# Kernel tuning notes

Hardware: AMD Instinct MI355X
Metric: run time of the kernel (lower is better)

The kernel has to match this reference:

```python
import jax, jax.numpy as jnp
import numpy as np

N = 100000      # nodes
E = 1600000     # edges (avg degree 16)
EP = 500000     # pos/neg scored edges
DIN, DH, DOUT = 128, 128, 64


def setup_inputs() -> dict:
    key = jax.random.key(0)
    ks = jax.random.split(key, 8)
    x = jax.random.normal(ks[0], (N, DIN), jnp.float32)
    edge_index = jax.random.randint(ks[1], (2, E), 0, N)
    pos_edge_index = jax.random.randint(ks[2], (2, EP), 0, N)
    neg_edge_index = jax.random.randint(ks[3], (2, EP), 0, N)
    s = lambda k, sh: jax.random.normal(k, sh, jnp.float32) * 0.05
    return dict(
        x=x, edge_index=edge_index,
        pos_edge_index=pos_edge_index, neg_edge_index=neg_edge_index,
        W_l0=s(ks[4], (DIN, DH)), b_l0=jnp.zeros((DH,), jnp.float32), W_r0=s(ks[5], (DIN, DH)),
        W_l1=s(ks[6], (DH, DOUT)), b_l1=jnp.zeros((DOUT,), jnp.float32), W_r1=s(ks[7], (DH, DOUT)),
    )


def sage_conv(h, src, dst, W_l, b_l, W_r):
    # PyG SAGEConv (mean aggr): out_i = W_l @ mean_{j in N(i)} h_j + b_l + W_r @ h_i
    msg = h[src]                                                   # [E, d] gather
    agg = jax.ops.segment_sum(msg, dst, num_segments=h.shape[0])   # [N, d]
    deg = jax.ops.segment_sum(jnp.ones((src.shape[0],), h.dtype), dst, num_segments=h.shape[0])
    mean = agg / jnp.maximum(deg, 1.0)[:, None]
    return mean @ W_l + b_l + h @ W_r


def reference(x, edge_index, pos_edge_index, neg_edge_index,
              W_l0, b_l0, W_r0, W_l1, b_l1, W_r1):
    src, dst = edge_index[0], edge_index[1]
    h = sage_conv(x, src, dst, W_l0, b_l0, W_r0)
    h = jax.nn.relu(h)          # dropout is identity in eval mode
    h = sage_conv(h, src, dst, W_l1, b_l1, W_r1)
    pos_scores = (h[pos_edge_index[0]] * h[pos_edge_index[1]]).sum(axis=1)
    neg_scores = (h[neg_edge_index[0]] * h[neg_edge_index[1]]).sum(axis=1)
    return (pos_scores, neg_scores)
```

## Files before the change

### kernel.cpp

```cpp
#include <hip/hip_runtime.h>

#define NN 100000
#define EE 1600000
#define EPE 500000
#define NBINS 196
#define BCAP 12288
#define EPB 2048
#define NB1 782
#define GEMMB 782
#define CONVB 6250

typedef short bf8_t __attribute__((ext_vector_type(8)));
typedef float f4_t  __attribute__((ext_vector_type(4)));
typedef float f2v  __attribute__((ext_vector_type(2)));

__device__ __forceinline__ unsigned short f2bf(float f) {
    unsigned u = __float_as_uint(f);
    unsigned r = (u + 0x7fffu + ((u >> 16) & 1u)) >> 16;
    return (unsigned short)r;
}
__device__ __forceinline__ float bfl(unsigned u) { return __uint_as_float(u << 16); }
__device__ __forceinline__ float bfh(unsigned u) { return __uint_as_float(u & 0xffff0000u); }

__device__ __forceinline__ int c0p(int m) {
    return ((m >> 6) & 1) * 64 + (m & 3) * 16 + ((m >> 2) & 15);
}
__device__ __forceinline__ int c1p(int m) {
    return ((m >> 5) & 1) * 32 + (m & 1) * 16 + ((m >> 1) & 15);
}

#if __has_builtin(__builtin_amdgcn_cvt_pk_fp8_f32) && __has_builtin(__builtin_amdgcn_cvt_pk_f32_fp8)
__device__ __forceinline__ unsigned pk4_fp8(float a0, float a1, float a2, float a3) {
    int w = 0;
    w = __builtin_amdgcn_cvt_pk_fp8_f32(a0, a1, w, false);
    w = __builtin_amdgcn_cvt_pk_fp8_f32(a2, a3, w, true);
    return (unsigned)w;
}
__device__ __forceinline__ unsigned short pk2_fp8(float a0, float a1) {
    int w = __builtin_amdgcn_cvt_pk_fp8_f32(a0, a1, 0, false);
    return (unsigned short)(w & 0xffff);
}
__device__ __forceinline__ void accf8(float* a, uint2 v) {
    f2v p0 = __builtin_amdgcn_cvt_pk_f32_fp8((int)v.x, false);
    f2v p1 = __builtin_amdgcn_cvt_pk_f32_fp8((int)v.x, true);
    f2v p2 = __builtin_amdgcn_cvt_pk_f32_fp8((int)v.y, false);
    f2v p3 = __builtin_amdgcn_cvt_pk_f32_fp8((int)v.y, true);
    a[0] += p0.x; a[1] += p0.y; a[2] += p1.x; a[3] += p1.y;
    a[4] += p2.x; a[5] += p2.y; a[6] += p3.x; a[7] += p3.y;
}
#else
#include <hip/hip_fp8.h>
__device__ __forceinline__ unsigned pk4_fp8(float a0, float a1, float a2, float a3) {
    unsigned r;
    r  = (unsigned)__hip_cvt_float_to_fp8(a0, __HIP_SATFINITE, __HIP_E4M3);
    r |= (unsigned)__hip_cvt_float_to_fp8(a1, __HIP_SATFINITE, __HIP_E4M3) << 8;
    r |= (unsigned)__hip_cvt_float_to_fp8(a2, __HIP_SATFINITE, __HIP_E4M3) << 16;
    r |= (unsigned)__hip_cvt_float_to_fp8(a3, __HIP_SATFINITE, __HIP_E4M3) << 24;
    return r;
}
__device__ __forceinline__ unsigned short pk2_fp8(float a0, float a1) {
    unsigned r;
    r  = (unsigned)__hip_cvt_float_to_fp8(a0, __HIP_SATFINITE, __HIP_E4M3);
    r |= (unsigned)__hip_cvt_float_to_fp8(a1, __HIP_SATFINITE, __HIP_E4M3) << 8;
    return (unsigned short)r;
}
__device__ __forceinline__ float dec1_fp8(unsigned b) {
    __hip_fp8_e4m3 h; h.__x = (__hip_fp8_storage_t)(b & 0xff);
    return (float)h;
}
__device__ __forceinline__ void accf8(float* a, uint2 v) {
    a[0] += dec1_fp8(v.x); a[1] += dec1_fp8(v.x >> 8);
    a[2] += dec1_fp8(v.x >> 16); a[3] += dec1_fp8(v.x >> 24);
    a[4] += dec1_fp8(v.y); a[5] += dec1_fp8(v.y >> 8);
    a[6] += dec1_fp8(v.y >> 16); a[7] += dec1_fp8(v.y >> 24);
}
#endif

__device__ void binpass1_body(int blk, const int* __restrict__ src,
                              const int* __restrict__ dst,
                              int* __restrict__ bin_cnt, int* __restrict__ binbuf)
{
    __shared__ int cnt_l[NBINS];
    __shared__ int base_l[NBINS];
    int tid = threadIdx.x;
    int e0 = blk * EPB;
    for (int i = tid; i < NBINS; i += 256) cnt_l[i] = 0;
    __syncthreads();

    int pk[8];
    #pragma unroll
    for (int i = 0; i < 8; ++i) {
        int e = e0 + tid + i * 256;
        pk[i] = -1;
        if (e < EE) {
            int d = dst[e];
            int b = d >> 9;
            int r = atomicAdd(&cnt_l[b], 1);
            pk[i] = (b << 20) | ((d & 511) << 11) | r;
        }
    }
    __syncthreads();
    for (int i = tid; i < NBINS; i += 256)
        base_l[i] = atomicAdd(&bin_cnt[i], cnt_l[i]);
    __syncthreads();

    #pragma unroll
    for (int i = 0; i < 8; ++i) {
        int e = e0 + tid + i * 256;
        if (e >= EE) continue;
        int v = pk[i];
        int b = v >> 20, dl = (v >> 11) & 511, r = v & 2047;
        binbuf[b * BCAP + base_l[b] + r] = (dl << 17) | src[e];
    }
}

__device__ void binpass2_body(int b, const int* __restrict__ binbuf,
                              const int* __restrict__ bin_cnt, int* __restrict__ csr,
                              int* __restrict__ row_ptr, float* __restrict__ invd)
{
    __shared__ int deg_l[512];
    __shared__ int off_l[512];
    __shared__ int cur_l[512];
    __shared__ int s[256];
    int tid = threadIdx.x;
    int lo = b << 9;
    int n_here = min(512, NN - lo);

    int bc = (tid < NBINS) ? bin_cnt[tid] : 0;
    s[tid] = bc;
    __syncthreads();
    #pragma unroll
    for (int off = 1; off < 256; off <<= 1) {
        int t = (tid >= off) ? s[tid - off] : 0;
        __syncthreads();
        s[tid] += t;
        __syncthreads();
    }
    int base = (b == 0) ? 0 : s[b - 1];
    int cnt = bin_cnt[b];
    const int* bb = binbuf + b * BCAP;
    __syncthreads();

    deg_l[tid] = 0; deg_l[tid + 256] = 0;
    __syncthreads();
    for (int i = tid; i < cnt; i += 256)
        atomicAdd(&deg_l[bb[i] >> 17], 1);
    __syncthreads();

    int a0 = deg_l[2 * tid], a1 = deg_l[2 * tid + 1];
    s[tid] = a0 + a1;
    __syncthreads();
    #pragma unroll
    for (int off = 1; off < 256; off <<= 1) {
        int t = (tid >= off) ? s[tid - off] : 0;
        __syncthreads();
        s[tid] += t;
        __syncthreads();
    }
    int excl = s[tid] - (a0 + a1);
    off_l[2 * tid] = excl;
    off_l[2 * tid + 1] = excl + a0;
    cur_l[2 * tid] = excl;
    cur_l[2 * tid + 1] = excl + a0;
    __syncthreads();

    for (int j = tid; j < n_here; j += 256) {
        row_ptr[lo + j] = base + off_l[j];
        invd[lo + j] = 1.0f / fmaxf((float)deg_l[j], 1.0f);
    }
    if (tid == 0 && b == NBINS - 1) row_ptr[NN] = EE;

    for (int i = tid; i < cnt; i += 256) {
        int v = bb[i];
        int dstl = v >> 17, srcv = v & 0x1FFFF;
        int pos = atomicAdd(&cur_l[dstl], 1);
        csr[base + pos] = srcv;
    }
}

__device__ void pack_body(int blk, const float* __restrict__ Wl0, const float* __restrict__ Wr0,
                          const float* __restrict__ Wl1, const float* __restrict__ Wr1,
                          const float* __restrict__ bl0, const float* __restrict__ bl1,
                          unsigned short* __restrict__ Bp0, unsigned short* __restrict__ Bp1,
                          float* __restrict__ b0p, float* __restrict__ b1p)
{
    int t = blk * 256 + threadIdx.x;
    if (t < 4096) {
        int q = t & 3;
        int n = (t >> 2) & 255;
        int kt = t >> 10;
        unsigned short o[8];
        #pragma unroll
        for (int j = 0; j < 8; ++j) {
            int k = kt * 32 + q * 8 + j;
            float v = (n < 128) ? Wl0[(size_t)k * 128 + n] : Wr0[(size_t)k * 128 + (n - 128)];
            o[j] = f2bf(v);
        }
        uint4 w;
        w.x = (unsigned)o[0] | ((unsigned)o[1] << 16);
        w.y = (unsigned)o[2] | ((unsigned)o[3] << 16);
        w.z = (unsigned)o[4] | ((unsigned)o[5] << 16);
        w.w = (unsigned)o[6] | ((unsigned)o[7] << 16);
        *(uint4*)(Bp0 + (size_t)t * 8) = w;
    } else if (t < 6144) {
        int u = t - 4096;
        int q = u & 3;
        int n = (u >> 2) & 127;
        int kt = u >> 9;
        unsigned short o[8];
        #pragma unroll
        for (int j = 0; j < 8; ++j) {
            int k = kt * 32 + q * 8 + j;
            int c = c0p(k);
            float v = (n < 64) ? Wl1[(size_t)c * 64 + n] : Wr1[(size_t)c * 64 + (n - 64)];
            o[j] = f2bf(v);
        }
        uint4 w;
        w.x = (unsigned)o[0] | ((unsigned)o[1] << 16);
        w.y = (unsigned)o[2] | ((unsigned)o[3] << 16);
        w.z = (unsigned)o[4] | ((unsigned)o[5] << 16);
        w.w = (unsigned)o[6] | ((unsigned)o[7] << 16);
        *(uint4*)(Bp1 + (size_t)u * 8) = w;
    } else if (t < 6144 + 128) {
        int m = t - 6144;
        b0p[m] = bl0[c0p(m)];
    } else if (t < 6144 + 192) {
        int m = t - 6272;
        b1p[m] = bl1[c1p(m)];
    }
}

__device__ void conv_body(int blk, const float* __restrict__ x, unsigned short* __restrict__ xb)
{
    int i = blk * 256 + threadIdx.x;
    const float4* xp = (const float4*)x + (size_t)i * 2;
    float4 a = xp[0], b = xp[1];
    uint4 w;
    w.x = (unsigned)f2bf(a.x) | ((unsigned)f2bf(a.y) << 16);
    w.y = (unsigned)f2bf(a.z) | ((unsigned)f2bf(a.w) << 16);
    w.z = (unsigned)f2bf(b.x) | ((unsigned)f2bf(b.y) << 16);
    w.w = (unsigned)f2bf(b.z) | ((unsigned)f2bf(b.w) << 16);
    *(uint4*)(xb + (size_t)i * 8) = w;
}

template<int NCOLS>
__device__ __forceinline__ void gemm_body(
    int blk, const unsigned short* __restrict__ Ab, const unsigned short* __restrict__ Bp,
    unsigned char* __restrict__ Tout, unsigned short* __restrict__ Rout)
{
    constexpr int STRIP = NCOLS / 4;
    constexpr int NT = STRIP / 16;
    constexpr int HC = NCOLS / 2;
    int w = threadIdx.x >> 6;
    int lane = threadIdx.x & 63;
    int ln = lane & 15, q = lane >> 4;
    int half = w >> 1, wsub = w & 1;
    int row0 = blk * 128;
    int colbase = half * HC + wsub * STRIP;

    bf8_t Bf[4][NT];
    #pragma unroll
    for (int kt = 0; kt < 4; ++kt)
        #pragma unroll
        for (int nt = 0; nt < NT; ++nt)
            Bf[kt][nt] = *(const bf8_t*)(Bp + (size_t)kt * NCOLS * 32
                                         + (size_t)(colbase + nt * 16 + ln) * 32 + q * 8);

    #pragma unroll
    for (int rt = 0; rt < 8; ++rt) {
        int rowt = row0 + rt * 16;
        if (rowt < NN) {
            int arow = rowt + ln;
            bf8_t Af[4];
            #pragma unroll
            for (int kt = 0; kt < 4; ++kt)
                Af[kt] = *(const bf8_t*)(Ab + (size_t)arow * 128 + kt * 32 + q * 8);

            f4_t acc[NT];
            #pragma unroll
            for (int nt = 0; nt < NT; ++nt) acc[nt] = (f4_t){0.f, 0.f, 0.f, 0.f};
            #pragma unroll
            for (int kt = 0; kt < 4; ++kt)
                #pragma unroll
                for (int nt = 0; nt < NT; ++nt)
                    acc[nt] = __builtin_amdgcn_mfma_f32_16x16x32_bf16(Af[kt], Bf[kt][nt], acc[nt], 0, 0, 0);

            #pragma unroll
            for (int r = 0; r < 4; ++r) {
                int row = rowt + q * 4 + r;
                if (half == 0) {
                    if (NT == 4) {
                        unsigned v = pk4_fp8(acc[0][r], acc[1][r], acc[2][r], acc[3][r]);
                        *(unsigned*)(Tout + (size_t)row * HC + wsub * 64 + ln * 4) = v;
                    } else {
                        unsigned short v = pk2_fp8(acc[0][r], acc[1][r]);
                        *(unsigned short*)(Tout + (size_t)row * HC + wsub * 32 + ln * 2) = v;
                    }
                } else {
                    if (NT == 4) {
                        uint2 v;
                        v.x = (unsigned)f2bf(acc[0][r]) | ((unsigned)f2bf(acc[1][r]) << 16);
                        v.y = (unsigned)f2bf(acc[2][r]) | ((unsigned)f2bf(acc[3][r]) << 16);
                        *(uint2*)(Rout + (size_t)row * HC + wsub * 64 + ln * 4) = v;
                    } else {
                        unsigned v = (unsigned)f2bf(acc[0][r]) | ((unsigned)f2bf(acc[1][r]) << 16);
                        *(unsigned*)(Rout + (size_t)row * HC + wsub * 32 + ln * 2) = v;
                    }
                }
            }
        }
    }
}

__global__ __launch_bounds__(256) void prep_k(
    const int* __restrict__ src, const int* __restrict__ dst,
    int* __restrict__ bin_cnt, int* __restrict__ binbuf,
    const float* __restrict__ x, unsigned short* __restrict__ xb,
    const float* __restrict__ Wl0, const float* __restrict__ Wr0,
    const float* __restrict__ Wl1, const float* __restrict__ Wr1,
    const float* __restrict__ bl0, const float* __restrict__ bl1,
    unsigned short* __restrict__ Bp0, unsigned short* __restrict__ Bp1,
    float* __restrict__ b0p, float* __restrict__ b1p)
{
    if (blockIdx.x < NB1)
        binpass1_body(blockIdx.x, src, dst, bin_cnt, binbuf);
    else if (blockIdx.x < NB1 + 25)
        pack_body(blockIdx.x - NB1, Wl0, Wr0, Wl1, Wr1, bl0, bl1, Bp0, Bp1, b0p, b1p);
    else
        conv_body(blockIdx.x - NB1 - 25, x, xb);
}

__global__ __launch_bounds__(256) void gemm0_bp2_k(
    const unsigned short* __restrict__ xb, const unsigned short* __restrict__ Bp0,
    unsigned char* __restrict__ t0q, unsigned short* __restrict__ r0b,
    const int* __restrict__ binbuf, const int* __restrict__ bin_cnt,
    int* __restrict__ csr, int* __restrict__ row_ptr, float* __restrict__ invd)
{
    if (blockIdx.x < GEMMB)
        gemm_body<256>(blockIdx.x, xb, Bp0, t0q, r0b);
    else
        binpass2_body(blockIdx.x - GEMMB, binbuf, bin_cnt, csr, row_ptr, invd);
}

__global__ __launch_bounds__(256) void gemm1_k(
    const unsigned short* __restrict__ h1b, const unsigned short* __restrict__ Bp1,
    unsigned char* __restrict__ t1q, unsigned short* __restrict__ r1b)
{
    gemm_body<128>(blockIdx.x, h1b, Bp1, t1q, r1b);
}

__device__ __forceinline__ void unp8(float* a, uint4 v) {
    a[0] = bfl(v.x); a[1] = bfh(v.x);
    a[2] = bfl(v.y); a[3] = bfh(v.y);
    a[4] = bfl(v.z); a[5] = bfh(v.z);
    a[6] = bfl(v.w); a[7] = bfh(v.w);
}

template<int LPNS, bool RELU>
__global__ __launch_bounds__(256) void gather_fuse_k(
    const unsigned char* __restrict__ tq, const int* __restrict__ csr,
    const int* __restrict__ row_ptr, const float* __restrict__ invd,
    const unsigned short* __restrict__ rg, const float* __restrict__ biasp,
    unsigned short* __restrict__ hout)
{
    constexpr int STRIDE = 8 << LPNS;
    int t = blockIdx.x * 256 + threadIdx.x;
    int node = t >> LPNS;
    int lane = t & ((1 << LPNS) - 1);
    if (node >= NN) return;
    int e = row_ptr[node];
    int e1 = row_ptr[node + 1];
    const unsigned char* fb = tq + lane * 8;

    float a0[8] = {0.f, 0.f, 0.f, 0.f, 0.f, 0.f, 0.f, 0.f};
    float a1[8] = {0.f, 0.f, 0.f, 0.f, 0.f, 0.f, 0.f, 0.f};
    for (; e + 3 < e1; e += 4) {
        int s0 = csr[e], s1 = csr[e + 1], s2 = csr[e + 2], s3 = csr[e + 3];
        uint2 v0 = *(const uint2*)(fb + (size_t)s0 * STRIDE);
        uint2 v1 = *(const uint2*)(fb + (size_t)s1 * STRIDE);
        uint2 v2 = *(const uint2*)(fb + (size_t)s2 * STRIDE);
        uint2 v3 = *(const uint2*)(fb + (size_t)s3 * STRIDE);
        accf8(a0, v0); accf8(a1, v1); accf8(a0, v2); accf8(a1, v3);
    }
    for (; e < e1; ++e) {
        int s0 = csr[e];
        uint2 v0 = *(const uint2*)(fb + (size_t)s0 * STRIDE);
        accf8(a0, v0);
    }

    float inv = invd[node];
    uint4 rv = *(const uint4*)(rg + (size_t)node * STRIDE + lane * 8);
    float rr[8];
    unp8(rr, rv);
    f4_t b0 = *(const f4_t*)(biasp + lane * 8);
    f4_t b1 = *(const f4_t*)(biasp + lane * 8 + 4);
    float o[8];
    #pragma unroll
    for (int j = 0; j < 8; ++j) {
        float bj = (j < 4) ? b0[j] : b1[j - 4];
        float v = (a0[j] + a1[j]) * inv + rr[j] + bj;
        o[j] = RELU ? fmaxf(v, 0.f) : v;
    }
    uint4 w;
    w.x = (unsigned)f2bf(o[0]) | ((unsigned)f2bf(o[1]) << 16);
    w.y = (unsigned)f2bf(o[2]) | ((unsigned)f2bf(o[3]) << 16);
    w.z = (unsigned)f2bf(o[4]) | ((unsigned)f2bf(o[5]) << 16);
    w.w = (unsigned)f2bf(o[6]) | ((unsigned)f2bf(o[7]) << 16);
    *(uint4*)(hout + (size_t)node * STRIDE + lane * 8) = w;
}

__device__ __forceinline__ float dot8(uint4 va, uint4 vb) {
    return bfl(va.x) * bfl(vb.x) + bfh(va.x) * bfh(vb.x)
         + bfl(va.y) * bfl(vb.y) + bfh(va.y) * bfh(vb.y)
         + bfl(va.z) * bfl(vb.z) + bfh(va.z) * bfh(vb.z)
         + bfl(va.w) * bfl(vb.w) + bfh(va.w) * bfh(vb.w);
}

__global__ __launch_bounds__(256) void score_k(
    const unsigned short* __restrict__ h2b, const int* __restrict__ pos,
    const int* __restrict__ neg, float* __restrict__ out)
{
    int t = blockIdx.x * 256 + threadIdx.x;
    int g = t >> 3, l = t & 7;
    int eg0 = g * 2;
    if (eg0 >= 2 * EPE) return;
    int eg1 = eg0 + 1;
    int a0i, b0i, a1i, b1i;
    if (eg0 < EPE) { a0i = pos[eg0]; b0i = pos[EPE + eg0]; }
    else { int e2 = eg0 - EPE; a0i = neg[e2]; b0i = neg[EPE + e2]; }
    if (eg1 < EPE) { a1i = pos[eg1]; b1i = pos[EPE + eg1]; }
    else { int e2 = eg1 - EPE; a1i = neg[e2]; b1i = neg[EPE + e2]; }
    const unsigned short* hb = h2b + (size_t)l * 8;
    uint4 va0 = *(const uint4*)(hb + (size_t)a0i * 64);
    uint4 vb0 = *(const uint4*)(hb + (size_t)b0i * 64);
    uint4 va1 = *(const uint4*)(hb + (size_t)a1i * 64);
    uint4 vb1 = *(const uint4*)(hb + (size_t)b1i * 64);
    float p0 = dot8(va0, vb0);
    float p1 = dot8(va1, vb1);
    p0 += __shfl_xor(p0, 1, 8);
    p1 += __shfl_xor(p1, 1, 8);
    p0 += __shfl_xor(p0, 2, 8);
    p1 += __shfl_xor(p1, 2, 8);
    p0 += __shfl_xor(p0, 4, 8);
    p1 += __shfl_xor(p1, 4, 8);
    if (l == 0) { out[eg0] = p0; out[eg1] = p1; }
}

extern "C" void kernel_launch(void* const* d_in, const int* in_sizes, int n_in,
                              void* d_out, int out_size, void* d_ws, size_t ws_size,
                              hipStream_t stream) {
    const float* x   = (const float*)d_in[0];
    const int*   ei  = (const int*)d_in[1];
    const int*   pei = (const int*)d_in[2];
    const int*   nei = (const int*)d_in[3];
    const float* Wl0 = (const float*)d_in[4];
    const float* bl0 = (const float*)d_in[5];
    const float* Wr0 = (const float*)d_in[6];
    const float* Wl1 = (const float*)d_in[7];
    const float* bl1 = (const float*)d_in[8];
    const float* Wr1 = (const float*)d_in[9];
    float* out = (float*)d_out;

    char* ws = (char*)d_ws;
    size_t off = 0;
    auto alloc = [&](size_t bytes) {
        void* p = ws + off;
        off = (off + bytes + 255) & ~(size_t)255;
        return p;
    };
    float* invd     = (float*)alloc((size_t)NN * 4);
    int*   row_ptr  = (int*)  alloc((size_t)(NN + 1) * 4);
    int*   bin_cnt  = (int*)  alloc((size_t)NBINS * 4);
    int*   binbuf   = (int*)  alloc((size_t)NBINS * BCAP * 4);
    int*   csr      = (int*)  alloc((size_t)EE * 4);
    unsigned short* Bp0 = (unsigned short*)alloc((size_t)4096 * 8 * 2);
    unsigned short* Bp1 = (unsigned short*)alloc((size_t)2048 * 8 * 2);
    float* b0p = (float*)alloc(128 * 4);
    float* b1p = (float*)alloc(64 * 4);
    unsigned short* xb  = (unsigned short*)alloc((size_t)NN * 128 * 2);
    unsigned char*  t0q = (unsigned char*) alloc((size_t)NN * 128);
    unsigned short* r0b = (unsigned short*)alloc((size_t)NN * 128 * 2);
    unsigned short* h1b = (unsigned short*)alloc((size_t)NN * 128 * 2);
    unsigned char*  t1q = t0q;
    unsigned short* r1b = r0b;
    unsigned short* h2b = h1b;

    const int* src = ei;
    const int* dst = ei + EE;

    hipMemsetAsync(bin_cnt, 0, (size_t)NBINS * 4, stream);

    prep_k<<<NB1 + 25 + CONVB, 256, 0, stream>>>(
        src, dst, bin_cnt, binbuf, x, xb,
        Wl0, Wr0, Wl1, Wr1, bl0, bl1, Bp0, Bp1, b0p, b1p);

    gemm0_bp2_k<<<GEMMB + NBINS, 256, 0, stream>>>(
        xb, Bp0, t0q, r0b, binbuf, bin_cnt, csr, row_ptr, invd);

    gather_fuse_k<4, true><<<(NN * 16 + 255) / 256, 256, 0, stream>>>(
        t0q, csr, row_ptr, invd, r0b, b0p, h1b);

    gemm1_k<<<GEMMB, 256, 0, stream>>>(h1b, Bp1, t1q, r1b);

    gather_fuse_k<3, false><<<(NN * 8 + 255) / 256, 256, 0, stream>>>(
        t1q, csr, row_ptr, invd, r1b, b1p, h2b);

    score_k<<<(EPE * 8 + 255) / 256, 256, 0, stream>>>(h2b, pei, nei, out);
}
```

Baseline: 284.3 us.

## Widen per-thread work in gather, binning and bf16 conversion kernels

The gather-fuse kernel now has each thread handle 16 features with 16-byte fp8 loads instead of 8 features with 8-byte loads. That halves the threads per node and the redundant CSR index reads, and makes each gather load wider. The binning pass now processes 4096 edges per block with a wider rank field, and the x-to-bf16 conversion handles 32 elements per thread, which shrinks the grid sizes. In exchange, per-thread register use rises, which can lower occupancy and latency hiding for the irregular gathers.

```diff
diff --git a/kernel.cpp b/kernel.cpp
--- a/kernel.cpp
+++ b/kernel.cpp
@@ -5,10 +5,10 @@
 #define EPE 500000
 #define NBINS 196
 #define BCAP 12288
-#define EPB 2048
-#define NB1 782
+#define EPB 4096
+#define NB1 391
 #define GEMMB 782
-#define CONVB 6250
+#define CONVB 1563
 
 typedef short bf8_t __attribute__((ext_vector_type(8)));
 typedef float f4_t  __attribute__((ext_vector_type(4)));
@@ -40,11 +40,11 @@
     int w = __builtin_amdgcn_cvt_pk_fp8_f32(a0, a1, 0, false);
     return (unsigned short)(w & 0xffff);
 }
-__device__ __forceinline__ void accf8(float* a, uint2 v) {
-    f2v p0 = __builtin_amdgcn_cvt_pk_f32_fp8((int)v.x, false);
-    f2v p1 = __builtin_amdgcn_cvt_pk_f32_fp8((int)v.x, true);
-    f2v p2 = __builtin_amdgcn_cvt_pk_f32_fp8((int)v.y, false);
-    f2v p3 = __builtin_amdgcn_cvt_pk_f32_fp8((int)v.y, true);
+__device__ __forceinline__ void accf8(float* a, unsigned lo, unsigned hi) {
+    f2v p0 = __builtin_amdgcn_cvt_pk_f32_fp8((int)lo, false);
+    f2v p1 = __builtin_amdgcn_cvt_pk_f32_fp8((int)lo, true);
+    f2v p2 = __builtin_amdgcn_cvt_pk_f32_fp8((int)hi, false);
+    f2v p3 = __builtin_amdgcn_cvt_pk_f32_fp8((int)hi, true);
     a[0] += p0.x; a[1] += p0.y; a[2] += p1.x; a[3] += p1.y;
     a[4] += p2.x; a[5] += p2.y; a[6] += p3.x; a[7] += p3.y;
 }
@@ -68,11 +68,11 @@
     __hip_fp8_e4m3 h; h.__x = (__hip_fp8_storage_t)(b & 0xff);
     return (float)h;
 }
-__device__ __forceinline__ void accf8(float* a, uint2 v) {
-    a[0] += dec1_fp8(v.x); a[1] += dec1_fp8(v.x >> 8);
-    a[2] += dec1_fp8(v.x >> 16); a[3] += dec1_fp8(v.x >> 24);
-    a[4] += dec1_fp8(v.y); a[5] += dec1_fp8(v.y >> 8);
-    a[6] += dec1_fp8(v.y >> 16); a[7] += dec1_fp8(v.y >> 24);
+__device__ __forceinline__ void accf8(float* a, unsigned lo, unsigned hi) {
+    a[0] += dec1_fp8(lo); a[1] += dec1_fp8(lo >> 8);
+    a[2] += dec1_fp8(lo >> 16); a[3] += dec1_fp8(lo >> 24);
+    a[4] += dec1_fp8(hi); a[5] += dec1_fp8(hi >> 8);
+    a[6] += dec1_fp8(hi >> 16); a[7] += dec1_fp8(hi >> 24);
 }
 #endif
 
@@ -87,16 +87,16 @@
     for (int i = tid; i < NBINS; i += 256) cnt_l[i] = 0;
     __syncthreads();
 
-    int pk[8];
-    #pragma unroll
-    for (int i = 0; i < 8; ++i) {
+    int pk[16];
+    #pragma unroll
+    for (int i = 0; i < 16; ++i) {
         int e = e0 + tid + i * 256;
         pk[i] = -1;
         if (e < EE) {
             int d = dst[e];
             int b = d >> 9;
             int r = atomicAdd(&cnt_l[b], 1);
-            pk[i] = (b << 20) | ((d & 511) << 11) | r;
+            pk[i] = (b << 21) | ((d & 511) << 12) | r;
         }
     }
     __syncthreads();
@@ -105,11 +105,11 @@
     __syncthreads();
 
     #pragma unroll
-    for (int i = 0; i < 8; ++i) {
+    for (int i = 0; i < 16; ++i) {
         int e = e0 + tid + i * 256;
         if (e >= EE) continue;
         int v = pk[i];
-        int b = v >> 20, dl = (v >> 11) & 511, r = v & 2047;
+        int b = v >> 21, dl = (v >> 12) & 511, r = v & 4095;
         binbuf[b * BCAP + base_l[b] + r] = (dl << 17) | src[e];
     }
 }
@@ -233,14 +233,22 @@
 __device__ void conv_body(int blk, const float* __restrict__ x, unsigned short* __restrict__ xb)
 {
     int i = blk * 256 + threadIdx.x;
-    const float4* xp = (const float4*)x + (size_t)i * 2;
-    float4 a = xp[0], b = xp[1];
-    uint4 w;
-    w.x = (unsigned)f2bf(a.x) | ((unsigned)f2bf(a.y) << 16);
-    w.y = (unsigned)f2bf(a.z) | ((unsigned)f2bf(a.w) << 16);
-    w.z = (unsigned)f2bf(b.x) | ((unsigned)f2bf(b.y) << 16);
-    w.w = (unsigned)f2bf(b.z) | ((unsigned)f2bf(b.w) << 16);
-    *(uint4*)(xb + (size_t)i * 8) = w;
+    if (i >= (NN * 128) / 32) return;
+    const float4* xp = (const float4*)x + (size_t)i * 8;
+    float4 v[8];
+    #pragma unroll
+    for (int j = 0; j < 8; ++j) v[j] = xp[j];
+    uint4* op = (uint4*)(xb + (size_t)i * 32);
+    #pragma unroll
+    for (int j = 0; j < 4; ++j) {
+        float4 a = v[2 * j], b = v[2 * j + 1];
+        uint4 w;
+        w.x = (unsigned)f2bf(a.x) | ((unsigned)f2bf(a.y) << 16);
+        w.y = (unsigned)f2bf(a.z) | ((unsigned)f2bf(a.w) << 16);
+        w.z = (unsigned)f2bf(b.x) | ((unsigned)f2bf(b.y) << 16);
+        w.w = (unsigned)f2bf(b.z) | ((unsigned)f2bf(b.w) << 16);
+        op[j] = w;
+    }
 }
 
 template<int NCOLS>
@@ -356,57 +364,69 @@
     a[6] = bfl(v.w); a[7] = bfh(v.w);
 }
 
-template<int LPNS, bool RELU>
+template<int LPNS2, bool RELU>
 __global__ __launch_bounds__(256) void gather_fuse_k(
     const unsigned char* __restrict__ tq, const int* __restrict__ csr,
     const int* __restrict__ row_ptr, const float* __restrict__ invd,
     const unsigned short* __restrict__ rg, const float* __restrict__ biasp,
     unsigned short* __restrict__ hout)
 {
-    constexpr int STRIDE = 8 << LPNS;
+    constexpr int ROW = 16 << LPNS2;
     int t = blockIdx.x * 256 + threadIdx.x;
-    int node = t >> LPNS;
-    int lane = t & ((1 << LPNS) - 1);
+    int node = t >> LPNS2;
+    int lane = t & ((1 << LPNS2) - 1);
     if (node >= NN) return;
     int e = row_ptr[node];
     int e1 = row_ptr[node + 1];
-    const unsigned char* fb = tq + lane * 8;
-
-    float a0[8] = {0.f, 0.f, 0.f, 0.f, 0.f, 0.f, 0.f, 0.f};
-    float a1[8] = {0.f, 0.f, 0.f, 0.f, 0.f, 0.f, 0.f, 0.f};
+    const unsigned char* fb = tq + lane * 16;
+
+    float a0[16], a1[16];
+    #pragma unroll
+    for (int j = 0; j < 16; ++j) { a0[j] = 0.f; a1[j] = 0.f; }
+
     for (; e + 3 < e1; e += 4) {
         int s0 = csr[e], s1 = csr[e + 1], s2 = csr[e + 2], s3 = csr[e + 3];
-        uint2 v0 = *(const uint2*)(fb + (size_t)s0 * STRIDE);
-        uint2 v1 = *(const uint2*)(fb + (size_t)s1 * STRIDE);
-        uint2 v2 = *(const uint2*)(fb + (size_t)s2 * STRIDE);
-        uint2 v3 = *(const uint2*)(fb + (size_t)s3 * STRIDE);
-        accf8(a0, v0); accf8(a1, v1); accf8(a0, v2); accf8(a1, v3);
+        uint4 v0 = *(const uint4*)(fb + (size_t)s0 * ROW);
+        uint4 v1 = *(const uint4*)(fb + (size_t)s1 * ROW);
+        uint4 v2 = *(const uint4*)(fb + (size_t)s2 * ROW);
+        uint4 v3 = *(const uint4*)(fb + (size_t)s3 * ROW);
+        accf8(a0, v0.x, v0.y); accf8(a0 + 8, v0.z, v0.w);
+        accf8(a1, v1.x, v1.y); accf8(a1 + 8, v1.z, v1.w);
+        accf8(a0, v2.x, v2.y); accf8(a0 + 8, v2.z, v2.w);
+        accf8(a1, v3.x, v3.y); accf8(a1 + 8, v3.z, v3.w);
     }
     for (; e < e1; ++e) {
         int s0 = csr[e];
-        uint2 v0 = *(const uint2*)(fb + (size_t)s0 * STRIDE);
-        accf8(a0, v0);
+        uint4 v0 = *(const uint4*)(fb + (size_t)s0 * ROW);
+        accf8(a0, v0.x, v0.y); accf8(a0 + 8, v0.z, v0.w);
     }
 
     float inv = invd[node];
-    uint4 rv = *(const uint4*)(rg + (size_t)node * STRIDE + lane * 8);
-    float rr[8];
-    unp8(rr, rv);
-    f4_t b0 = *(const f4_t*)(biasp + lane * 8);
-    f4_t b1 = *(const f4_t*)(biasp + lane * 8 + 4);
-    float o[8];
-    #pragma unroll
-    for (int j = 0; j < 8; ++j) {
-        float bj = (j < 4) ? b0[j] : b1[j - 4];
-        float v = (a0[j] + a1[j]) * inv + rr[j] + bj;
+    const unsigned short* rp = rg + (size_t)node * ROW + lane * 16;
+    uint4 rv0 = *(const uint4*)rp;
+    uint4 rv1 = *(const uint4*)(rp + 8);
+    float rr[16];
+    unp8(rr, rv0); unp8(rr + 8, rv1);
+    const float* bp = biasp + lane * 16;
+
+    float o[16];
+    #pragma unroll
+    for (int j = 0; j < 16; ++j) {
+        float v = (a0[j] + a1[j]) * inv + rr[j] + bp[j];
         o[j] = RELU ? fmaxf(v, 0.f) : v;
     }
-    uint4 w;
-    w.x = (unsigned)f2bf(o[0]) | ((unsigned)f2bf(o[1]) << 16);
-    w.y = (unsigned)f2bf(o[2]) | ((unsigned)f2bf(o[3]) << 16);
-    w.z = (unsigned)f2bf(o[4]) | ((unsigned)f2bf(o[5]) << 16);
-    w.w = (unsigned)f2bf(o[6]) | ((unsigned)f2bf(o[7]) << 16);
-    *(uint4*)(hout + (size_t)node * STRIDE + lane * 8) = w;
+    uint4 w0, w1;
+    w0.x = (unsigned)f2bf(o[0])  | ((unsigned)f2bf(o[1])  << 16);
+    w0.y = (unsigned)f2bf(o[2])  | ((unsigned)f2bf(o[3])  << 16);
+    w0.z = (unsigned)f2bf(o[4])  | ((unsigned)f2bf(o[5])  << 16);
+    w0.w = (unsigned)f2bf(o[6])  | ((unsigned)f2bf(o[7])  << 16);
+    w1.x = (unsigned)f2bf(o[8])  | ((unsigned)f2bf(o[9])  << 16);
+    w1.y = (unsigned)f2bf(o[10]) | ((unsigned)f2bf(o[11]) << 16);
+    w1.z = (unsigned)f2bf(o[12]) | ((unsigned)f2bf(o[13]) << 16);
+    w1.w = (unsigned)f2bf(o[14]) | ((unsigned)f2bf(o[15]) << 16);
+    unsigned short* op = hout + (size_t)node * ROW + lane * 16;
+    *(uint4*)op = w0;
+    *(uint4*)(op + 8) = w1;
 }
 
 __device__ __forceinline__ float dot8(uint4 va, uint4 vb) {
@@ -497,12 +517,12 @@
     gemm0_bp2_k<<<GEMMB + NBINS, 256, 0, stream>>>(
         xb, Bp0, t0q, r0b, binbuf, bin_cnt, csr, row_ptr, invd);
 
-    gather_fuse_k<4, true><<<(NN * 16 + 255) / 256, 256, 0, stream>>>(
+    gather_fuse_k<3, true><<<(NN * 8 + 255) / 256, 256, 0, stream>>>(
         t0q, csr, row_ptr, invd, r0b, b0p, h1b);
 
     gemm1_k<<<GEMMB, 256, 0, stream>>>(h1b, Bp1, t1q, r1b);
 
-    gather_fuse_k<3, false><<<(NN * 8 + 255) / 256, 256, 0, stream>>>(
+    gather_fuse_k<2, false><<<(NN * 4 + 255) / 256, 256, 0, stream>>>(
         t1q, csr, row_ptr, invd, r1b, b1p, h2b);
 
     score_k<<<(EPE * 8 + 255) / 256, 256, 0, stream>>>(h2b, pei, nei, out);
```

Result: no change. 280.9 us (-1.2%).
